# Optimization experiments

Hardware: AMD Instinct MI355X
Metric: run time of the kernel (lower is better)

## Reference

```python
import jax, jax.numpy as jnp
import numpy as np

B, LQ, LKV = 4, 512, 4096
IN_DIM, N_HEADS, DIM_HEAD = 1024, 16, 64
INNER = N_HEADS * DIM_HEAD


def setup_inputs() -> dict:
    key = jax.random.key(0)
    ks = jax.random.split(key, 6)
    q = jax.random.normal(ks[0], (B, LQ, IN_DIM), dtype=jnp.float32)
    kv = jax.random.normal(ks[1], (B, LKV, IN_DIM), dtype=jnp.float32)
    mask = jax.random.randint(ks[2], (B, 1, 1, LKV), 0, 2).astype(jnp.bool_)
    w_scale = 0.02
    Wq = jax.random.normal(ks[3], (IN_DIM, INNER), dtype=jnp.float32) * w_scale
    Wkv = jax.random.normal(ks[4], (IN_DIM, 2 * INNER), dtype=jnp.float32) * w_scale
    Wo = jax.random.normal(ks[5], (INNER, IN_DIM), dtype=jnp.float32) * w_scale
    return {"q": q, "kv": kv, "mask": mask, "Wq": Wq, "Wkv": Wkv, "Wo": Wo}


def reference(q, kv, mask, Wq, Wkv, Wo):
    # projections
    qp = q @ Wq                                  # [B, LQ, INNER]
    kvp = kv @ Wkv                               # [B, LKV, 2*INNER]
    # split heads
    qh = qp.reshape(B, LQ, N_HEADS, DIM_HEAD).transpose(0, 2, 1, 3)   # [B,H,LQ,D]
    kvh = kvp.reshape(B, LKV, N_HEADS, 2 * DIM_HEAD).transpose(0, 2, 1, 3)
    kh, vh = kvh[..., :DIM_HEAD], kvh[..., DIM_HEAD:]                 # [B,H,LKV,D]
    scale = jnp.sqrt(jnp.asarray(DIM_HEAD, dtype=qh.dtype))
    scores = jnp.einsum("bhqd,bhkd->bhqk", qh, kh) / scale            # [B,H,LQ,LKV]
    scores = jnp.where(mask, -jnp.inf, scores)
    weights = jax.nn.softmax(scores, axis=-1)
    context = jnp.einsum("bhqk,bhkd->bhqd", weights, vh)              # [B,H,LQ,D]
    context = context.transpose(0, 2, 1, 3).reshape(B, LQ, INNER)
    return context @ Wo                                               # [B,LQ,IN_DIM]
```

## Files before the change

kernel.cpp:

```cpp
#include <hip/hip_runtime.h>
#include <hip/hip_bf16.h>
#include <math.h>

#define B_      4
#define LQ_     512
#define LKV_    4096
#define IN_DIM_ 1024
#define NH_     16
#define DH_     64
#define INNER_  1024

typedef _Float16 f16x8 __attribute__((ext_vector_type(8)));
typedef _Float16 f16x4 __attribute__((ext_vector_type(4)));
typedef float    f32x4 __attribute__((ext_vector_type(4)));

#define GLDS(gp, lp) __builtin_amdgcn_global_load_lds( \
    (const __attribute__((address_space(1))) void*)(gp), \
    (__attribute__((address_space(3))) void*)(lp), 16, 0, 0)

__global__ __launch_bounds__(256) void scan_mask(const int* __restrict__ mask,
                                                 int* __restrict__ pidx,
                                                 int* __restrict__ cnt) {
  __shared__ int wsum_s[4];
  int b = blockIdx.x, tid = threadIdx.x;
  const int* mb = mask + b * LKV_;
  int base = tid * 16;
  int vals[16];
#pragma unroll
  for (int i = 0; i < 4; ++i) {
    int4 v = *(const int4*)(mb + base + i * 4);
    vals[i * 4 + 0] = v.x; vals[i * 4 + 1] = v.y;
    vals[i * 4 + 2] = v.z; vals[i * 4 + 3] = v.w;
  }
  int s = 0;
#pragma unroll
  for (int j = 0; j < 16; ++j) s += (vals[j] == 0);
  int lane = tid & 63, wave = tid >> 6;
  int inc = s;
#pragma unroll
  for (int d = 1; d < 64; d <<= 1) {
    int v = __shfl_up(inc, d);
    if (lane >= d) inc += v;
  }
  if (lane == 63) wsum_s[wave] = inc;
  __syncthreads();
  int woff = 0;
#pragma unroll
  for (int w = 0; w < 4; ++w)
    if (w < wave) woff += wsum_s[w];
  if (tid == 255) cnt[b] = woff + inc;
  int run = woff + inc - s;
#pragma unroll
  for (int i = 0; i < 4; ++i) {
    int4 o;
    int* op = &o.x;
#pragma unroll
    for (int j = 0; j < 4; ++j) { op[j] = run; run += (vals[i * 4 + j] == 0); }
    *(int4*)(pidx + b * LKV_ + base + i * 4) = o;
  }
}

__device__ __forceinline__ void transpose_tile(const float* __restrict__ in,
                                               _Float16* __restrict__ out,
                                               int K, int N, int xb, int yb,
                                               float (*t)[33]) {
  int bn = xb * 32, bk = yb * 32;
  int tx = threadIdx.x & 31, ty = threadIdx.x >> 5;
#pragma unroll
  for (int i = 0; i < 4; ++i) {
    int r = ty + i * 8;
    t[r][tx] = in[(size_t)(bk + r) * N + bn + tx];
  }
  __syncthreads();
#pragma unroll
  for (int i = 0; i < 4; ++i) {
    int r = ty + i * 8;
    out[(size_t)(bn + r) * K + bk + tx] = (_Float16)t[tx][r];
  }
}

__global__ __launch_bounds__(256) void prep_compact(
    const float* __restrict__ kv, const float* __restrict__ q,
    const float* __restrict__ Wq, const float* __restrict__ Wkv,
    const float* __restrict__ Wo, const int* __restrict__ mask,
    const int* __restrict__ pidx,
    _Float16* __restrict__ kv16, _Float16* __restrict__ q16,
    _Float16* __restrict__ Wqt, _Float16* __restrict__ Wkvt,
    _Float16* __restrict__ Wot) {
  __shared__ float t[32][33];
  const int id = blockIdx.x, tid = threadIdx.x;
  if (id < 16384) {
    if (mask[id] != 0) return;
    int b = id >> 12;
    int dst = b * LKV_ + pidx[id];
    float4 v = ((const float4*)(kv + (size_t)id * IN_DIM_))[tid];
    f16x4 h = {(_Float16)v.x, (_Float16)v.y, (_Float16)v.z, (_Float16)v.w};
    ((f16x4*)(kv16 + (size_t)dst * IN_DIM_))[tid] = h;
  } else if (id < 18432) {
    int i = (id - 16384) * 256 + tid;
    float4 v = ((const float4*)q)[i];
    f16x4 h = {(_Float16)v.x, (_Float16)v.y, (_Float16)v.z, (_Float16)v.w};
    ((f16x4*)q16)[i] = h;
  } else if (id < 19456) {
    int l = id - 18432;
    transpose_tile(Wq, Wqt, 1024, 1024, l & 31, l >> 5, t);
  } else if (id < 21504) {
    int l = id - 19456;
    transpose_tile(Wkv, Wkvt, 1024, 2048, l & 63, l >> 6, t);
  } else {
    int l = id - 21504;
    transpose_tile(Wo, Wot, 1024, 1024, l & 31, l >> 5, t);
  }
}

__global__ __launch_bounds__(256, 4) void proj_f16(
    const _Float16* __restrict__ kv16, const _Float16* __restrict__ Wkvt,
    const _Float16* __restrict__ q16, const _Float16* __restrict__ Wqt,
    _Float16* __restrict__ qp16, _Float16* __restrict__ Kp,
    _Float16* __restrict__ Vt, const int* __restrict__ Cnt) {
  const int id = blockIdx.x;
  const bool is_kv = (id < 2048);
  int brow, bcol;
  const _Float16 *Ab, *Bb;
  if (is_kv) {
    bcol = (id & 15) * 128;
    brow = (id >> 4) * 128;
    if ((brow & 4095) >= Cnt[brow >> 12]) return;
    Ab = kv16 + (size_t)brow * 1024;
    Bb = Wkvt + (size_t)bcol * 1024;
  } else {
    int l = id - 2048;
    bcol = (l & 7) * 128;
    brow = (l >> 3) * 128;
    Ab = q16 + (size_t)brow * 1024;
    Bb = Wqt + (size_t)bcol * 1024;
  }
  __shared__ _Float16 As[128 * 64];
  __shared__ _Float16 Bs[128 * 64];
  const int tid = threadIdx.x;
  const int wave = tid >> 6, lane = tid & 63;
  const int quad = lane >> 4, l16 = lane & 15;
  const int wm = (wave & 1) * 64, wn = (wave >> 1) * 64;
  const int ro8 = lane >> 3, c8 = lane & 7;

  f32x4 acc[4][4];
#pragma unroll
  for (int i = 0; i < 4; ++i)
#pragma unroll
    for (int j = 0; j < 4; ++j) acc[i][j] = (f32x4){0.f, 0.f, 0.f, 0.f};

  for (int k0 = 0; k0 < 1024; k0 += 64) {
    __syncthreads();
#pragma unroll
    for (int i = 0; i < 4; ++i) {
      int rbase = wave * 32 + i * 8;
      int row = rbase + ro8;
      int g = c8 ^ (row & 7);
      GLDS(Ab + (size_t)row * 1024 + k0 + g * 8, &As[rbase * 64]);
      GLDS(Bb + (size_t)row * 1024 + k0 + g * 8, &Bs[rbase * 64]);
    }
    __syncthreads();
#pragma unroll
    for (int ks = 0; ks < 2; ++ks) {
      f16x8 af[4], bf[4];
      int c = ks * 4 + quad;
#pragma unroll
      for (int mt = 0; mt < 4; ++mt) {
        int r = wm + mt * 16 + l16;
        af[mt] = *(const f16x8*)&As[r * 64 + ((c ^ (r & 7)) * 8)];
        int rb = wn + mt * 16 + l16;
        bf[mt] = *(const f16x8*)&Bs[rb * 64 + ((c ^ (rb & 7)) * 8)];
      }
#pragma unroll
      for (int mt = 0; mt < 4; ++mt)
#pragma unroll
        for (int nt = 0; nt < 4; ++nt)
          acc[mt][nt] = __builtin_amdgcn_mfma_f32_16x16x32_f16(af[mt], bf[nt], acc[mt][nt], 0, 0, 0);
    }
  }

#pragma unroll
  for (int mt = 0; mt < 4; ++mt) {
    int row0 = brow + wm + mt * 16 + quad * 4;
#pragma unroll
    for (int nt = 0; nt < 4; ++nt) {
      int col = bcol + wn + nt * 16 + l16;
      f32x4 v = acc[mt][nt];
      if (is_kv) {
        int h = col >> 7, w64 = col & 63;
        if ((col & 127) < 64) {
#pragma unroll
          for (int r = 0; r < 4; ++r)
            Kp[(size_t)(row0 + r) * INNER_ + h * 64 + w64] = (_Float16)v[r];
        } else {
          int b = row0 >> 12, key = row0 & 4095;
          f16x4 pk = {(_Float16)v[0], (_Float16)v[1], (_Float16)v[2], (_Float16)v[3]};
          *(f16x4*)&Vt[((size_t)((b * NH_ + h) * DH_) + w64) * LKV_ + key] = pk;
        }
      } else {
#pragma unroll
        for (int r = 0; r < 4; ++r)
          qp16[(size_t)(row0 + r) * 1024 + col] = (_Float16)v[r];
      }
    }
  }
}

__global__ __launch_bounds__(256, 2) void attn_f16(
    const _Float16* __restrict__ qp, const _Float16* __restrict__ Kp,
    const _Float16* __restrict__ Vt, const int* __restrict__ cnt,
    float* __restrict__ opart, float* __restrict__ lpart) {
  const int idx = blockIdx.x;
  const int bh = idx & 63, qt = (idx >> 6) & 7, half = idx >> 9;
  const int b = bh >> 4, h = bh & 15;
  __shared__ _Float16 Ks[128 * 64];
  __shared__ _Float16 Vts[64 * 128];
  __shared__ _Float16 Pl[64][136];

  const int tid = threadIdx.x;
  const int wave = tid >> 6, lane = tid & 63;
  const int quad = lane >> 4, l16 = lane & 15;
  const int ro8 = lane >> 3, gch8 = (lane & 7) ^ (ro8 & 7);
  const int ro16 = lane >> 4, ch16 = lane & 15;

  const int qrow = b * LQ_ + qt * 64 + wave * 16 + l16;
  const _Float16* qpr = qp + (size_t)qrow * INNER_ + h * DH_;
  f16x8 qf[2];
  qf[0] = *(const f16x8*)(qpr + quad * 8);
  qf[1] = *(const f16x8*)(qpr + 32 + quad * 8);

  const int c_act = cnt[b];
  const int tiles = (c_act + 127) >> 7;
  const int htiles = (tiles + 1) >> 1;
  const int t0 = half * htiles;
  const int t1 = (half == 0) ? htiles : tiles;

  float l_run = 0.f;
  f32x4 oacc[4];
#pragma unroll
  for (int i = 0; i < 4; ++i) oacc[i] = (f32x4){0.f, 0.f, 0.f, 0.f};

  const _Float16* kb = Kp + (size_t)(b * LKV_) * INNER_ + h * DH_;
  const _Float16* vb = Vt + (size_t)((b * NH_ + h) * DH_) * LKV_;

  for (int t = t0; t < t1; ++t) {
    __syncthreads();
#pragma unroll
    for (int i = 0; i < 4; ++i) {
      int rbase = wave * 32 + i * 8;
      GLDS(kb + (size_t)(t * 128 + rbase + ro8) * INNER_ + gch8 * 8, &Ks[rbase * 64]);
    }
#pragma unroll
    for (int i = 0; i < 4; ++i) {
      int rbase = wave * 16 + i * 4;
      int row = rbase + ro16;
      int gch = ch16 ^ (row & 15);
      GLDS(vb + (size_t)row * LKV_ + t * 128 + gch * 8, &Vts[rbase * 128]);
    }
    __syncthreads();

    f32x4 sacc[8];
#pragma unroll
    for (int i = 0; i < 8; ++i) sacc[i] = (f32x4){0.f, 0.f, 0.f, 0.f};
#pragma unroll
    for (int ks = 0; ks < 2; ++ks) {
      int c = ks * 4 + quad;
#pragma unroll
      for (int mt = 0; mt < 8; ++mt) {
        int krow = mt * 16 + l16;
        f16x8 af = *(const f16x8*)&Ks[krow * 64 + ((c ^ (krow & 7)) * 8)];
        sacc[mt] = __builtin_amdgcn_mfma_f32_16x16x32_f16(af, qf[ks], sacc[mt], 0, 0, 0);
      }
    }
    const int lim = c_act - t * 128;
    float psloc = 0.f;
#pragma unroll
    for (int mt = 0; mt < 8; ++mt) {
      f16x4 pk;
#pragma unroll
      for (int r = 0; r < 4; ++r) {
        int key = mt * 16 + quad * 4 + r;
        float s = sacc[mt][r] * 0.125f;
        if (key >= lim) s = -1e30f;
        float p = __expf(s - 8.0f);
        psloc += p;
        pk[r] = (_Float16)p;
      }
      *(f16x4*)&Pl[wave * 16 + l16][mt * 16 + quad * 4] = pk;
    }
    psloc += __shfl_xor(psloc, 16);
    psloc += __shfl_xor(psloc, 32);
    l_run += psloc;
#pragma unroll
    for (int ks = 0; ks < 4; ++ks) {
      int c = ks * 4 + quad;
      f16x8 bf = *(const f16x8*)&Pl[wave * 16 + l16][ks * 32 + quad * 8];
#pragma unroll
      for (int mt = 0; mt < 4; ++mt) {
        int drow = mt * 16 + l16;
        f16x8 af = *(const f16x8*)&Vts[drow * 128 + ((c ^ (drow & 15)) * 8)];
        oacc[mt] = __builtin_amdgcn_mfma_f32_16x16x32_f16(af, bf, oacc[mt], 0, 0, 0);
      }
    }
  }

  float* ob = opart + ((size_t)(half * 2048 + qrow)) * INNER_ + h * DH_;
#pragma unroll
  for (int mt = 0; mt < 4; ++mt)
    *(f32x4*)(ob + mt * 16 + quad * 4) = oacc[mt];
  if (quad == 0) lpart[(size_t)(half * 2048 + qrow) * NH_ + h] = l_run;
}

__global__ __launch_bounds__(256) void attn_fin(const float* __restrict__ opart,
                                                const float* __restrict__ lpart,
                                                _Float16* __restrict__ ctx) {
  int row = blockIdx.x, t = threadIdx.x;
  int h = t >> 4;
  float l = lpart[(size_t)row * NH_ + h] + lpart[(size_t)(2048 + row) * NH_ + h];
  float inv = (l > 0.f) ? 1.f / l : 0.f;
  f32x4 a = *(const f32x4*)(opart + (size_t)row * INNER_ + t * 4);
  f32x4 c = *(const f32x4*)(opart + (size_t)(2048 + row) * INNER_ + t * 4);
  f16x4 o;
#pragma unroll
  for (int r = 0; r < 4; ++r) o[r] = (_Float16)((a[r] + c[r]) * inv);
  *(f16x4*)(ctx + (size_t)row * INNER_ + t * 4) = o;
}

__global__ __launch_bounds__(256, 2) void gemm_out(
    const _Float16* __restrict__ A, const _Float16* __restrict__ Bt,
    float* __restrict__ C) {
  const int brow = blockIdx.y * 64, bcol = blockIdx.x * 64;
  __shared__ _Float16 As[64 * 64];
  __shared__ _Float16 Bs[64 * 64];
  const int tid = threadIdx.x;
  const int wave = tid >> 6, lane = tid & 63;
  const int quad = lane >> 4, l16 = lane & 15;
  const int wm = (wave & 1) * 32, wn = (wave >> 1) * 32;
  const int ro8 = lane >> 3, c8 = lane & 7;

  f32x4 acc[2][2];
#pragma unroll
  for (int i = 0; i < 2; ++i)
#pragma unroll
    for (int j = 0; j < 2; ++j) acc[i][j] = (f32x4){0.f, 0.f, 0.f, 0.f};

  const _Float16* Ab = A + (size_t)brow * 1024;
  const _Float16* Bb = Bt + (size_t)bcol * 1024;

  for (int k0 = 0; k0 < 1024; k0 += 64) {
    __syncthreads();
#pragma unroll
    for (int i = 0; i < 2; ++i) {
      int rbase = wave * 16 + i * 8;
      int row = rbase + ro8;
      int g = c8 ^ (row & 7);
      GLDS(Ab + (size_t)row * 1024 + k0 + g * 8, &As[rbase * 64]);
      GLDS(Bb + (size_t)row * 1024 + k0 + g * 8, &Bs[rbase * 64]);
    }
    __syncthreads();
#pragma unroll
    for (int ks = 0; ks < 2; ++ks) {
      f16x8 af[2], bf[2];
      int c = ks * 4 + quad;
#pragma unroll
      for (int mt = 0; mt < 2; ++mt) {
        int r = wm + mt * 16 + l16;
        af[mt] = *(const f16x8*)&As[r * 64 + ((c ^ (r & 7)) * 8)];
        int rb = wn + mt * 16 + l16;
        bf[mt] = *(const f16x8*)&Bs[rb * 64 + ((c ^ (rb & 7)) * 8)];
      }
#pragma unroll
      for (int mt = 0; mt < 2; ++mt)
#pragma unroll
        for (int nt = 0; nt < 2; ++nt)
          acc[mt][nt] = __builtin_amdgcn_mfma_f32_16x16x32_f16(af[mt], bf[nt], acc[mt][nt], 0, 0, 0);
    }
  }

#pragma unroll
  for (int mt = 0; mt < 2; ++mt) {
    int row0 = brow + wm + mt * 16 + quad * 4;
#pragma unroll
    for (int nt = 0; nt < 2; ++nt) {
      int col = bcol + wn + nt * 16 + l16;
      f32x4 v = acc[mt][nt];
#pragma unroll
      for (int r = 0; r < 4; ++r) C[(size_t)(row0 + r) * 1024 + col] = v[r];
    }
  }
}

extern "C" void kernel_launch(void* const* d_in, const int* in_sizes, int n_in,
                              void* d_out, int out_size, void* d_ws, size_t ws_size,
                              hipStream_t stream) {
  const float* q   = (const float*)d_in[0];
  const float* kv  = (const float*)d_in[1];
  const int* mask  = (const int*)d_in[2];
  const float* Wq  = (const float*)d_in[3];
  const float* Wkv = (const float*)d_in[4];
  const float* Wo  = (const float*)d_in[5];
  float* out = (float*)d_out;

  _Float16* p = (_Float16*)d_ws;
  _Float16* q16   = p; p += (size_t)2048 * 1024;
  _Float16* kv16  = p; p += (size_t)16384 * 1024;
  _Float16* Wqt   = p; p += (size_t)1024 * 1024;
  _Float16* Wkvt  = p; p += (size_t)2048 * 1024;
  _Float16* Wot   = p; p += (size_t)1024 * 1024;
  _Float16* qp16  = p; p += (size_t)2048 * 1024;
  _Float16* Kp    = p; p += (size_t)16384 * 1024;
  _Float16* Vt    = p; p += (size_t)16384 * 1024;
  _Float16* ctx16 = p; p += (size_t)2048 * 1024;
  float* opart = (float*)p; p += (size_t)2 * 4096 * 1024;
  float* lpart = (float*)p; p += (size_t)2 * 2048 * NH_ * 2;
  int* pidx = (int*)p;
  int* cnt  = pidx + 16384;

  scan_mask<<<4, 256, 0, stream>>>(mask, pidx, cnt);
  prep_compact<<<22528, 256, 0, stream>>>(kv, q, Wq, Wkv, Wo, mask, pidx,
                                          kv16, q16, Wqt, Wkvt, Wot);
  proj_f16<<<2176, 256, 0, stream>>>(kv16, Wkvt, q16, Wqt, qp16, Kp, Vt, cnt);
  attn_f16<<<1024, 256, 0, stream>>>(qp16, Kp, Vt, cnt, opart, lpart);
  attn_fin<<<2048, 256, 0, stream>>>(opart, lpart, ctx16);
  gemm_out<<<dim3(16, 32), 256, 0, stream>>>(ctx16, Wot, out);
}
```

Baseline: 229.3 us.

## Remove split-KV attention and fuse normalization into attention kernel

Each attention block now processes all key tiles for its query tile instead of half, then normalizes by the running sum and writes f16 context directly. This eliminates the fp32 partial output/sum buffers and the separate finalize kernel launch. It halves the number of blocks, reducing available parallelism and load balancing across CUs.

New measurement: 233.8 us. About the same (+1.9%).

```diff
diff --git a/kernel.cpp b/kernel.cpp
--- a/kernel.cpp
+++ b/kernel.cpp
@@ -209,9 +209,9 @@
 __global__ __launch_bounds__(256, 2) void attn_f16(
     const _Float16* __restrict__ qp, const _Float16* __restrict__ Kp,
     const _Float16* __restrict__ Vt, const int* __restrict__ cnt,
-    float* __restrict__ opart, float* __restrict__ lpart) {
+    _Float16* __restrict__ ctx) {
   const int idx = blockIdx.x;
-  const int bh = idx & 63, qt = (idx >> 6) & 7, half = idx >> 9;
+  const int bh = idx & 63, qt = idx >> 6;
   const int b = bh >> 4, h = bh & 15;
   __shared__ _Float16 Ks[128 * 64];
   __shared__ _Float16 Vts[64 * 128];
@@ -231,9 +231,6 @@
 
   const int c_act = cnt[b];
   const int tiles = (c_act + 127) >> 7;
-  const int htiles = (tiles + 1) >> 1;
-  const int t0 = half * htiles;
-  const int t1 = (half == 0) ? htiles : tiles;
 
   float l_run = 0.f;
   f32x4 oacc[4];
@@ -243,7 +240,7 @@
   const _Float16* kb = Kp + (size_t)(b * LKV_) * INNER_ + h * DH_;
   const _Float16* vb = Vt + (size_t)((b * NH_ + h) * DH_) * LKV_;
 
-  for (int t = t0; t < t1; ++t) {
+  for (int t = 0; t < tiles; ++t) {
     __syncthreads();
 #pragma unroll
     for (int i = 0; i < 4; ++i) {
@@ -304,26 +301,15 @@
     }
   }
 
-  float* ob = opart + ((size_t)(half * 2048 + qrow)) * INNER_ + h * DH_;
-#pragma unroll
-  for (int mt = 0; mt < 4; ++mt)
-    *(f32x4*)(ob + mt * 16 + quad * 4) = oacc[mt];
-  if (quad == 0) lpart[(size_t)(half * 2048 + qrow) * NH_ + h] = l_run;
-}
-
-__global__ __launch_bounds__(256) void attn_fin(const float* __restrict__ opart,
-                                                const float* __restrict__ lpart,
-                                                _Float16* __restrict__ ctx) {
-  int row = blockIdx.x, t = threadIdx.x;
-  int h = t >> 4;
-  float l = lpart[(size_t)row * NH_ + h] + lpart[(size_t)(2048 + row) * NH_ + h];
-  float inv = (l > 0.f) ? 1.f / l : 0.f;
-  f32x4 a = *(const f32x4*)(opart + (size_t)row * INNER_ + t * 4);
-  f32x4 c = *(const f32x4*)(opart + (size_t)(2048 + row) * INNER_ + t * 4);
-  f16x4 o;
-#pragma unroll
-  for (int r = 0; r < 4; ++r) o[r] = (_Float16)((a[r] + c[r]) * inv);
-  *(f16x4*)(ctx + (size_t)row * INNER_ + t * 4) = o;
+  const float inv = (l_run > 0.f) ? 1.f / l_run : 0.f;
+  _Float16* cb = ctx + (size_t)qrow * INNER_ + h * DH_;
+#pragma unroll
+  for (int mt = 0; mt < 4; ++mt) {
+    f16x4 o;
+#pragma unroll
+    for (int r = 0; r < 4; ++r) o[r] = (_Float16)(oacc[mt][r] * inv);
+    *(f16x4*)(cb + mt * 16 + quad * 4) = o;
+  }
 }
 
 __global__ __launch_bounds__(256, 2) void gemm_out(
@@ -411,8 +397,6 @@
   _Float16* Kp    = p; p += (size_t)16384 * 1024;
   _Float16* Vt    = p; p += (size_t)16384 * 1024;
   _Float16* ctx16 = p; p += (size_t)2048 * 1024;
-  float* opart = (float*)p; p += (size_t)2 * 4096 * 1024;
-  float* lpart = (float*)p; p += (size_t)2 * 2048 * NH_ * 2;
   int* pidx = (int*)p;
   int* cnt  = pidx + 16384;
 
@@ -420,7 +404,6 @@
   prep_compact<<<22528, 256, 0, stream>>>(kv, q, Wq, Wkv, Wo, mask, pidx,
                                           kv16, q16, Wqt, Wkvt, Wot);
   proj_f16<<<2176, 256, 0, stream>>>(kv16, Wkvt, q16, Wqt, qp16, Kp, Vt, cnt);
-  attn_f16<<<1024, 256, 0, stream>>>(qp16, Kp, Vt, cnt, opart, lpart);
-  attn_fin<<<2048, 256, 0, stream>>>(opart, lpart, ctx16);
+  attn_f16<<<512, 256, 0, stream>>>(qp16, Kp, Vt, cnt, ctx16);
   gemm_out<<<dim3(16, 32), 256, 0, stream>>>(ctx16, Wot, out);
 }
```
